# Performance work log

Hardware: AMD Instinct MI355X
Metric: run time of the kernel (lower is better)

Reference implementation:

```python
import jax, jax.numpy as jnp
import numpy as np

WD = WH = WW = 7      # cubic window
NH = 3                # num_heads
RATE = 1              # idx == 1 -> rate = 1, num_heads_rate = 0
FF = 3.0              # focusing_factor (<= 6 branch)
EPS = 1e-6


def setup_inputs() -> dict:
    key = jax.random.key(0)
    ks = jax.random.split(key, 6)
    B, D, H, W, C = 1, 56, 56, 56, 96
    hd = C // NH
    x = jax.random.normal(ks[0], (B, D, H, W, C), dtype=jnp.float32)
    w_qkv = jax.random.normal(ks[1], (C, 3 * C), dtype=jnp.float32) * 0.02
    scale_param = jnp.zeros((RATE, 1, 1, hd), dtype=jnp.float32)
    pos_enc = jax.random.normal(ks[2], (RATE, 1, WD * WH * WW, hd), dtype=jnp.float32) * 0.02
    dwc_w = jax.random.normal(ks[3], (hd * RATE, 1, 5, 5, 5), dtype=jnp.float32) * 0.02
    dwc_b = jnp.zeros((hd * RATE,), dtype=jnp.float32)
    w_proj = jax.random.normal(ks[4], (C, C), dtype=jnp.float32) * 0.02
    b_proj = jnp.zeros((C,), dtype=jnp.float32)
    return {"x": x, "w_qkv": w_qkv, "scale_param": scale_param, "pos_enc": pos_enc,
            "dwc_w": dwc_w, "dwc_b": dwc_b, "w_proj": w_proj, "b_proj": b_proj}


def _forward(x, w_qkv, scale_param, pos_enc, dwc_w, dwc_b, w_proj, b_proj):
    B, D, H, W, C = x.shape
    hd = C // NH
    nD, nH_, nW_ = D // WD, H // WH, W // WW
    N = WD * WH * WW
    # qkv projection (no bias) -> (3, B, D, H, W, C)
    qkv = (x @ w_qkv).reshape(B, D, H, W, 3, C).transpose(4, 0, 1, 2, 3, 5)
    # window partition (rate == 1): (3, 1, B*nWin, N, C)
    qkv = qkv.reshape(3, B, nD, WD, nH_, WH, nW_, WW, C)
    qkv = qkv.transpose(0, 1, 2, 4, 6, 3, 5, 7, 8).reshape(3, RATE, B * nD * nH_ * nW_, N, C)
    q, k, v = qkv[0], qkv[1], qkv[2]

    def heads(t):  # 'r b n (h c) -> r (b h) n c'
        r, b, n, c0 = t.shape
        return t.reshape(r, b, n, NH, hd).transpose(0, 1, 3, 2, 4).reshape(r, b * NH, n, hd)

    q, k, v = heads(q), heads(k), heads(v)
    k = k + pos_enc
    scale = jax.nn.softplus(scale_param)
    q = (jax.nn.relu(q) + EPS) / scale
    k = (jax.nn.relu(k) + EPS) / scale
    qn = jnp.linalg.norm(q, axis=-1, keepdims=True)
    kn = jnp.linalg.norm(k, axis=-1, keepdims=True)
    q = q ** FF
    k = k ** FF
    q = q / jnp.linalg.norm(q, axis=-1, keepdims=True) * qn
    k = k / jnp.linalg.norm(k, axis=-1, keepdims=True) * kn
    # linear attention, kv-first branch (i*j*(c+d) > c*d*(i+j) for N=343, hd=32)
    z = 1.0 / (jnp.einsum('rbic,rbc->rbi', q, k.sum(axis=2)) + EPS)
    kv = jnp.einsum('rbjc,rbjd->rbcd', k, v)
    out = jnp.einsum('rbic,rbcd,rbi->rbid', q, kv, z)
    # depthwise 3D conv feature map on v: 'r b (d w h) c -> b (r c) d w h'
    r, b, n, c = v.shape
    fm = v.reshape(r, b, WD, WH, WW, c).transpose(1, 0, 5, 2, 3, 4).reshape(b, r * c, WD, WH, WW)
    fm = jax.lax.conv_general_dilated(fm, dwc_w, (1, 1, 1), [(2, 2)] * 3,
                                      dimension_numbers=('NCDHW', 'OIDHW', 'NCDHW'),
                                      feature_group_count=r * c)
    fm = fm + dwc_b[None, :, None, None, None]
    fm = fm.reshape(b, r, c, WD, WH, WW).transpose(1, 0, 3, 4, 5, 2).reshape(r, b, n, c)
    out = out + fm
    # merge heads: 'r (b h) n c -> r b n (h c)'
    Bw = b // NH
    out = out.reshape(r, Bw, NH, n, hd).transpose(0, 1, 3, 2, 4).reshape(r, Bw, n, C)
    # window reverse (rate == 1)
    out = out.reshape(B, nD, nH_, nW_, WD, WH, WW, C)
    out = out.transpose(0, 1, 4, 2, 5, 3, 6, 7).reshape(B, D, H, W, C)
    return out @ w_proj + b_proj


def reference(x, w_qkv, scale_param, pos_enc, dwc_w, dwc_b, w_proj, b_proj):
    return _forward(x, w_qkv, scale_param, pos_enc, dwc_w, dwc_b, w_proj, b_proj)
```

## Files before the change

### kernel.cpp

```cpp
#include <hip/hip_runtime.h>
#include <math.h>

#define NWIN 512
#define NHD  3
#define NTOK 343
#define HD   32
#define CH   96
#define DIM  56

#define XS 16.0f
#define WS 1024.0f
#define RS (1.0f/16384.0f)

typedef __attribute__((ext_vector_type(8))) _Float16 f16x8;
typedef __attribute__((ext_vector_type(4))) float f32x4;

__device__ __forceinline__ unsigned short f2h_bits(float x) {
    _Float16 h = (_Float16)x;
    return __builtin_bit_cast(unsigned short, h);
}
__device__ __forceinline__ float h2f_bits(unsigned short u) {
    return (float)__builtin_bit_cast(_Float16, u);
}
__device__ __forceinline__ f32x4 mfma16h(f16x8 a, f16x8 b, f32x4 c) {
    return __builtin_amdgcn_mfma_f32_16x16x32_f16(a, b, c, 0, 0, 0);
}
__device__ __forceinline__ float shfl16_sum(float v) {
    v += __shfl_xor(v, 1);
    v += __shfl_xor(v, 2);
    v += __shfl_xor(v, 4);
    v += __shfl_xor(v, 8);
    return v;
}

__global__ void setup_w(const float* __restrict__ w_qkv,
                        unsigned short* __restrict__ wsb)
{
    int i = blockIdx.x * 256 + threadIdx.x;
    if (i >= 108 * 512) return;
    int e = i & 7, l = (i >> 3) & 63;
    int fid = i >> 9;
    int hl = fid & 1; int f2 = fid >> 1;
    int ks = f2 % 3; int f3 = f2 / 3;
    int nt = f3 & 1; int f4 = f3 >> 1;
    int m  = f4 % 3; int h  = f4 / 3;
    int kg  = ks * 32 + (l >> 4) * 8 + e;
    int col = m * 96 + h * 32 + nt * 16 + (l & 15);
    float w = w_qkv[kg * 288 + col] * WS;
    unsigned short hi = f2h_bits(w);
    wsb[i] = hl ? f2h_bits(w - h2f_bits(hi)) : hi;
}

#define BUILD_AFRAG(AH, AL, XPTR)                                           \
  { _Pragma("unroll")                                                       \
    for (int ks = 0; ks < 3; ++ks) {                                        \
        float4 x0 = *(const float4*)((XPTR) + ks * 32);                     \
        float4 x1 = *(const float4*)((XPTR) + ks * 32 + 4);                 \
        union { _Float16 e[8]; f16x8 v; } th, tl;                           \
        float s[8] = {x0.x, x0.y, x0.z, x0.w, x1.x, x1.y, x1.z, x1.w};      \
        _Pragma("unroll")                                                   \
        for (int e = 0; e < 8; ++e) {                                       \
            float sv = s[e] * XS;                                           \
            unsigned short hi = f2h_bits(sv);                               \
            th.e[e] = __builtin_bit_cast(_Float16, hi);                     \
            tl.e[e] = (_Float16)(sv - h2f_bits(hi));                        \
        }                                                                   \
        AH[ks] = th.v; AL[ks] = tl.v;                                       \
    } }

__global__ __launch_bounds__(256, 4) void attn_kernel(
    const float* __restrict__ x, const unsigned short* __restrict__ wsb,
    const float* __restrict__ scale_param, const float* __restrict__ pos_enc,
    const float* __restrict__ dwc_w, const float* __restrict__ dwc_b,
    float* __restrict__ y)
{
    __shared__ __align__(16) unsigned short v16[352 * HD];
    __shared__ __align__(16) union UU {
        struct PA { unsigned short kf16c[64 * 34]; } pa;
        struct PB {
            unsigned short qfL[64 * 40];
            unsigned short kvS[32 * 40];
            float ksred[4][2][16];
        } pb;
        float dwc[HD * 125];
    } u;
    __shared__ float ksum_s[HD];
    __shared__ float sps[HD];

    const int tid = threadIdx.x, bid = blockIdx.x;
    const int h = bid >> 9, win = bid & 511;
    const int wd = win >> 6, wh = (win >> 3) & 7, ww = win & 7;
    const int wv = tid >> 6, lane = tid & 63;
    const int quad = lane >> 4, li = lane & 15;
    const int g8 = tid >> 5, c = tid & 31;
    const int mtw = wv >> 1, ntw = wv & 1;

    if (tid < HD) {
        float sv = scale_param[tid];
        sps[tid] = (sv > 20.f) ? sv : log1pf(expf(sv));
    }
    __syncthreads();
    const float sp0 = sps[li], sp1 = sps[16 + li];

    const f16x8* wf = (const f16x8*)wsb;
    const int fbase = h * 36;
    float ksp0 = 0.f, ksp1 = 0.f;
    f32x4 kvacc = {0.f, 0.f, 0.f, 0.f};

    for (int cb0 = 0; cb0 < NTOK; cb0 += 64) {
        const int nj = min(64, NTOK - cb0);
        int atok = cb0 + wv * 16 + li;
        int atc = min(atok, NTOK - 1);
        int adz = atc / 49, arem = atc - adz * 49, ady = arem / 7, adx = arem - ady * 7;
        int gA = ((wd * 7 + adz) * DIM + (wh * 7 + ady)) * DIM + (ww * 7 + adx);
        const float* xr = x + (size_t)gA * CH + quad * 8;
        f16x8 ah[3], al[3];
        BUILD_AFRAG(ah, al, xr);

        f32x4 ak[2] = {{0,0,0,0},{0,0,0,0}};
        f32x4 av[2] = {{0,0,0,0},{0,0,0,0}};
        #pragma unroll
        for (int nt = 0; nt < 2; ++nt) {
            #pragma unroll
            for (int ks = 0; ks < 3; ++ks) {
                int fk = (fbase + ((1 * 2 + nt) * 3 + ks) * 2) * 64 + lane;
                int fv = (fbase + ((2 * 2 + nt) * 3 + ks) * 2) * 64 + lane;
                f16x8 bkh = wf[fk], bkl = wf[fk + 64];
                f16x8 bvh = wf[fv];
                ak[nt] = mfma16h(ah[ks], bkh, ak[nt]);
                ak[nt] = mfma16h(ah[ks], bkl, ak[nt]);
                ak[nt] = mfma16h(al[ks], bkh, ak[nt]);
                av[nt] = mfma16h(ah[ks], bvh, av[nt]);
                av[nt] = mfma16h(al[ks], bvh, av[nt]);
            }
        }

        #pragma unroll
        for (int j = 0; j < 4; ++j) {
            int t16 = quad * 4 + j;
            int tok = cb0 + wv * 16 + t16;
            bool val = tok < NTOK;
            int tc = val ? tok : NTOK - 1;
            float pe0 = pos_enc[tc * HD + li];
            float pe1 = pos_enc[tc * HD + 16 + li];
            float kr0 = ak[0][j] * RS + pe0;
            float kr1 = ak[1][j] * RS + pe1;
            float kp0 = (fmaxf(kr0, 0.f) + 1e-6f) / sp0;
            float kp1 = (fmaxf(kr1, 0.f) + 1e-6f) / sp1;
            float k30 = kp0 * kp0 * kp0, k31 = kp1 * kp1 * kp1;
            float n2k = fmaf(kp0, kp0, kp1 * kp1);
            float n6k = fmaf(k30, k30, k31 * k31);
            n2k = shfl16_sum(n2k); n6k = shfl16_sum(n6k);
            float sk = sqrtf(n2k / n6k);
            float kf0 = k30 * sk, kf1 = k31 * sk;
            int tl = wv * 16 + t16;
            if (val) {
                ksp0 += kf0; ksp1 += kf1;
                u.pa.kf16c[tl * 34 + li]      = f2h_bits(kf0);
                u.pa.kf16c[tl * 34 + 16 + li] = f2h_bits(kf1);
                v16[tok * HD + li]      = f2h_bits(av[0][j] * RS);
                v16[tok * HD + 16 + li] = f2h_bits(av[1][j] * RS);
            } else {
                u.pa.kf16c[tl * 34 + li]      = 0;
                u.pa.kf16c[tl * 34 + 16 + li] = 0;
                if (tok < 352) {
                    v16[tok * HD + li]      = 0;
                    v16[tok * HD + 16 + li] = 0;
                }
            }
        }
        __syncthreads();

        const int nsteps = (nj + 31) >> 5;
        for (int s = 0; s < nsteps; ++s) {
            union { unsigned short u16a[8]; f16x8 v; } a8, b8;
            #pragma unroll
            for (int e = 0; e < 8; ++e) {
                int row = s * 32 + quad * 8 + e;
                a8.u16a[e] = u.pa.kf16c[row * 34 + mtw * 16 + li];
                b8.u16a[e] = v16[(cb0 + row) * HD + ntw * 16 + li];
            }
            kvacc = mfma16h(a8.v, b8.v, kvacc);
        }
        __syncthreads();
    }

    ksp0 += __shfl_xor(ksp0, 16); ksp0 += __shfl_xor(ksp0, 32);
    ksp1 += __shfl_xor(ksp1, 16); ksp1 += __shfl_xor(ksp1, 32);
    if (quad == 0) { u.pb.ksred[wv][0][li] = ksp0; u.pb.ksred[wv][1][li] = ksp1; }
    #pragma unroll
    for (int j = 0; j < 4; ++j)
        u.pb.kvS[(ntw * 16 + li) * 40 + mtw * 16 + quad * 4 + j] = f2h_bits(kvacc[j]);
    __syncthreads();
    if (tid < HD) {
        ksum_s[tid] = u.pb.ksred[0][tid >> 4][tid & 15] + u.pb.ksred[1][tid >> 4][tid & 15]
                    + u.pb.ksred[2][tid >> 4][tid & 15] + u.pb.ksred[3][tid >> 4][tid & 15];
    }
    __syncthreads();

    const float ks0 = ksum_s[li], ks1 = ksum_s[16 + li];
    for (int cb0 = 0; cb0 < NTOK; cb0 += 64) {
        int atok = cb0 + wv * 16 + li;
        int atc = min(atok, NTOK - 1);
        int adz = atc / 49, arem = atc - adz * 49, ady = arem / 7, adx = arem - ady * 7;
        int gA = ((wd * 7 + adz) * DIM + (wh * 7 + ady)) * DIM + (ww * 7 + adx);
        const float* xr = x + (size_t)gA * CH + quad * 8;
        f16x8 ah[3], al[3];
        BUILD_AFRAG(ah, al, xr);

        f32x4 aq[2] = {{0,0,0,0},{0,0,0,0}};
        #pragma unroll
        for (int nt = 0; nt < 2; ++nt) {
            #pragma unroll
            for (int ks = 0; ks < 3; ++ks) {
                int fq = (fbase + ((0 * 2 + nt) * 3 + ks) * 2) * 64 + lane;
                f16x8 bqh = wf[fq], bql = wf[fq + 64];
                aq[nt] = mfma16h(ah[ks], bqh, aq[nt]);
                aq[nt] = mfma16h(ah[ks], bql, aq[nt]);
                aq[nt] = mfma16h(al[ks], bqh, aq[nt]);
            }
        }

        float zq[4];
        #pragma unroll
        for (int j = 0; j < 4; ++j) {
            int t16 = quad * 4 + j;
            int tok = cb0 + wv * 16 + t16;
            bool val = tok < NTOK;
            float qp0 = (fmaxf(aq[0][j] * RS, 0.f) + 1e-6f) / sp0;
            float qp1 = (fmaxf(aq[1][j] * RS, 0.f) + 1e-6f) / sp1;
            float q30 = qp0 * qp0 * qp0, q31 = qp1 * qp1 * qp1;
            float n2q = fmaf(qp0, qp0, qp1 * qp1);
            float n6q = fmaf(q30, q30, q31 * q31);
            n2q = shfl16_sum(n2q); n6q = shfl16_sum(n6q);
            float sq = sqrtf(n2q / n6q);
            float qf0 = q30 * sq, qf1 = q31 * sq;
            float zp = shfl16_sum(fmaf(qf0, ks0, qf1 * ks1));
            zq[j] = 1.f / (zp + 1e-6f);
            if (val) {
                int tl = wv * 16 + t16;
                u.pb.qfL[tl * 40 + li]      = f2h_bits(qf0);
                u.pb.qfL[tl * 40 + 16 + li] = f2h_bits(qf1);
            }
        }
        f16x8 aqf = *(const f16x8*)&u.pb.qfL[(wv * 16 + li) * 40 + quad * 8];
        f16x8 bk0 = *(const f16x8*)&u.pb.kvS[li * 40 + quad * 8];
        f16x8 bk1 = *(const f16x8*)&u.pb.kvS[(16 + li) * 40 + quad * 8];
        f32x4 at0 = {0.f, 0.f, 0.f, 0.f}, at1 = {0.f, 0.f, 0.f, 0.f};
        at0 = mfma16h(aqf, bk0, at0);
        at1 = mfma16h(aqf, bk1, at1);

        #pragma unroll
        for (int j = 0; j < 4; ++j) {
            int t16 = quad * 4 + j;
            int tok = cb0 + wv * 16 + t16;
            if (tok < NTOK) {
                int dz = tok / 49, rem = tok - dz * 49, dy = rem / 7, dxx = rem - dy * 7;
                int g = ((wd * 7 + dz) * DIM + (wh * 7 + dy)) * DIM + (ww * 7 + dxx);
                y[(size_t)g * CH + h * HD + li]      = at0[j] * zq[j];
                y[(size_t)g * CH + h * HD + 16 + li] = at1[j] * zq[j];
            }
        }
    }

    __threadfence_block();
    __syncthreads();

    for (int i = tid; i < HD * 125; i += 256) u.dwc[i] = dwc_w[i];
    __syncthreads();

    const float bias_c = dwc_b[c];
    for (int it = g8; it < 49; it += 8) {
        int dz = it / 7, dy = it - dz * 7;
        float fm[7] = {0.f, 0.f, 0.f, 0.f, 0.f, 0.f, 0.f};
        #pragma unroll
        for (int ka2 = 0; ka2 < 5; ++ka2) {
            int za = dz + ka2 - 2;
            if ((unsigned)za >= 7u) continue;
            #pragma unroll
            for (int kb = 0; kb < 5; ++kb) {
                int zb = dy + kb - 2;
                if ((unsigned)zb >= 7u) continue;
                const unsigned short* vb = &v16[(za * 49 + zb * 7) * HD + c];
                float vr[7];
                #pragma unroll
                for (int xx = 0; xx < 7; ++xx) vr[xx] = h2f_bits(vb[xx * HD]);
                const float* wb = &u.dwc[c * 125 + ka2 * 25 + kb * 5];
                float w0 = wb[0], w1 = wb[1], w2 = wb[2], w3 = wb[3], w4 = wb[4];
                #pragma unroll
                for (int dx2 = 0; dx2 < 7; ++dx2) {
                    if (dx2 - 2 >= 0) fm[dx2] = fmaf(vr[dx2 - 2], w0, fm[dx2]);
                    if (dx2 - 1 >= 0) fm[dx2] = fmaf(vr[dx2 - 1], w1, fm[dx2]);
                    fm[dx2] = fmaf(vr[dx2], w2, fm[dx2]);
                    if (dx2 + 1 <= 6) fm[dx2] = fmaf(vr[dx2 + 1], w3, fm[dx2]);
                    if (dx2 + 2 <= 6) fm[dx2] = fmaf(vr[dx2 + 2], w4, fm[dx2]);
                }
            }
        }
        int tokbase = ((wd * 7 + dz) * DIM + (wh * 7 + dy)) * DIM + ww * 7;
        #pragma unroll
        for (int dx2 = 0; dx2 < 7; ++dx2) {
            float* yp = &y[(size_t)(tokbase + dx2) * CH + h * HD + c];
            *yp += fm[dx2] + bias_c;
        }
    }
}

__global__ __launch_bounds__(512, 1) void proj_kernel(
    const float* __restrict__ wp, const float* __restrict__ bp,
    float* __restrict__ y)
{
    __shared__ float yt[256 * 97];
    __shared__ float wl[96 * 96];

    const int tid = threadIdx.x;
    const int base = blockIdx.x * 256;

    for (int i = tid; i < 96 * 96; i += 512) wl[i] = wp[i];
    for (int i = tid; i < 256 * 96; i += 512) {
        int r = i / 96; int ch2 = i - r * 96;
        yt[r * 97 + ch2] = y[(base + r) * 96 + ch2];
    }
    __syncthreads();

    const int tokg = tid & 127;
    const int outg = tid >> 7;

    float acc[2][24];
    #pragma unroll
    for (int jj = 0; jj < 24; ++jj) {
        float b = bp[outg * 24 + jj];
        acc[0][jj] = b; acc[1][jj] = b;
    }

    for (int cc = 0; cc < 96; ++cc) {
        float y0 = yt[(tokg)       * 97 + cc];
        float y1 = yt[(tokg + 128) * 97 + cc];
        const float* wrow = &wl[cc * 96 + outg * 24];
        #pragma unroll
        for (int jj = 0; jj < 24; ++jj) {
            float wvv = wrow[jj];
            acc[0][jj] = fmaf(y0, wvv, acc[0][jj]);
            acc[1][jj] = fmaf(y1, wvv, acc[1][jj]);
        }
    }
    __syncthreads();

    #pragma unroll
    for (int i = 0; i < 2; ++i) {
        int tok = base + tokg + 128 * i;
        #pragma unroll
        for (int jj = 0; jj < 24; ++jj)
            y[tok * 96 + outg * 24 + jj] = acc[i][jj];
    }
}

extern "C" void kernel_launch(void* const* d_in, const int* in_sizes, int n_in,
                              void* d_out, int out_size, void* d_ws, size_t ws_size,
                              hipStream_t stream) {
    const float* x           = (const float*)d_in[0];
    const float* w_qkv       = (const float*)d_in[1];
    const float* scale_param = (const float*)d_in[2];
    const float* pos_enc     = (const float*)d_in[3];
    const float* dwc_w       = (const float*)d_in[4];
    const float* dwc_b       = (const float*)d_in[5];
    const float* w_proj      = (const float*)d_in[6];
    const float* b_proj      = (const float*)d_in[7];
    float* out = (float*)d_out;
    unsigned short* wsb = (unsigned short*)d_ws;

    setup_w<<<dim3(216), dim3(256), 0, stream>>>(w_qkv, wsb);
    attn_kernel<<<dim3(NHD * NWIN), dim3(256), 0, stream>>>(
        x, wsb, scale_param, pos_enc, dwc_w, dwc_b, out);
    proj_kernel<<<dim3(686), dim3(512), 0, stream>>>(w_proj, b_proj, out);
}
```

Measured before the change: 292.4 us.

## Run output projection on MFMA with split-f16 weights prepacked in setup

```diff
diff --git a/kernel.cpp b/kernel.cpp
--- a/kernel.cpp
+++ b/kernel.cpp
@@ -11,6 +11,8 @@
 #define XS 16.0f
 #define WS 1024.0f
 #define RS (1.0f/16384.0f)
+#define YS 4.0f
+#define RSP (1.0f/4096.0f)
 
 typedef __attribute__((ext_vector_type(8))) _Float16 f16x8;
 typedef __attribute__((ext_vector_type(4))) float f32x4;
@@ -34,24 +36,40 @@
 }
 
 __global__ void setup_w(const float* __restrict__ w_qkv,
+                        const float* __restrict__ w_proj,
                         unsigned short* __restrict__ wsb)
 {
     int i = blockIdx.x * 256 + threadIdx.x;
-    if (i >= 108 * 512) return;
+    if (i >= 144 * 512) return;
     int e = i & 7, l = (i >> 3) & 63;
-    int fid = i >> 9;
-    int hl = fid & 1; int f2 = fid >> 1;
-    int ks = f2 % 3; int f3 = f2 / 3;
-    int nt = f3 & 1; int f4 = f3 >> 1;
-    int m  = f4 % 3; int h  = f4 / 3;
-    int kg  = ks * 32 + (l >> 4) * 8 + e;
-    int col = m * 96 + h * 32 + nt * 16 + (l & 15);
-    float w = w_qkv[kg * 288 + col] * WS;
-    unsigned short hi = f2h_bits(w);
-    wsb[i] = hl ? f2h_bits(w - h2f_bits(hi)) : hi;
-}
-
-#define BUILD_AFRAG(AH, AL, XPTR)                                           \
+    int kg, col; const float* src;
+    int fid;
+    if (i < 108 * 512) {
+        fid = i >> 9;
+        int hl = fid & 1; int f2 = fid >> 1;
+        int ks = f2 % 3; int f3 = f2 / 3;
+        int nt = f3 & 1; int f4 = f3 >> 1;
+        int m  = f4 % 3; int h  = f4 / 3;
+        kg  = ks * 32 + (l >> 4) * 8 + e;
+        col = m * 96 + h * 32 + nt * 16 + (l & 15);
+        src = w_qkv; 
+        float w = src[kg * 288 + col] * WS;
+        unsigned short hi = f2h_bits(w);
+        wsb[i] = (fid & 1) ? f2h_bits(w - h2f_bits(hi)) : hi;
+    } else {
+        int i2 = i - 108 * 512;
+        fid = i2 >> 9;
+        int hl = fid & 1; int f2 = fid >> 1;
+        int ks = f2 % 3; int nt = f2 / 3;
+        kg  = ks * 32 + (l >> 4) * 8 + e;
+        col = nt * 16 + (l & 15);
+        float w = w_proj[kg * 96 + col] * WS;
+        unsigned short hi = f2h_bits(w);
+        wsb[i] = hl ? f2h_bits(w - h2f_bits(hi)) : hi;
+    }
+}
+
+#define BUILD_AFRAG_S(AH, AL, XPTR, SCALE)                                  \
   { _Pragma("unroll")                                                       \
     for (int ks = 0; ks < 3; ++ks) {                                        \
         float4 x0 = *(const float4*)((XPTR) + ks * 32);                     \
@@ -60,7 +78,7 @@
         float s[8] = {x0.x, x0.y, x0.z, x0.w, x1.x, x1.y, x1.z, x1.w};      \
         _Pragma("unroll")                                                   \
         for (int e = 0; e < 8; ++e) {                                       \
-            float sv = s[e] * XS;                                           \
+            float sv = s[e] * (SCALE);                                      \
             unsigned short hi = f2h_bits(sv);                               \
             th.e[e] = __builtin_bit_cast(_Float16, hi);                     \
             tl.e[e] = (_Float16)(sv - h2f_bits(hi));                        \
@@ -115,7 +133,7 @@
         int gA = ((wd * 7 + adz) * DIM + (wh * 7 + ady)) * DIM + (ww * 7 + adx);
         const float* xr = x + (size_t)gA * CH + quad * 8;
         f16x8 ah[3], al[3];
-        BUILD_AFRAG(ah, al, xr);
+        BUILD_AFRAG_S(ah, al, xr, XS);
 
         f32x4 ak[2] = {{0,0,0,0},{0,0,0,0}};
         f32x4 av[2] = {{0,0,0,0},{0,0,0,0}};
@@ -206,7 +224,7 @@
         int gA = ((wd * 7 + adz) * DIM + (wh * 7 + ady)) * DIM + (ww * 7 + adx);
         const float* xr = x + (size_t)gA * CH + quad * 8;
         f16x8 ah[3], al[3];
-        BUILD_AFRAG(ah, al, xr);
+        BUILD_AFRAG_S(ah, al, xr, XS);
 
         f32x4 aq[2] = {{0,0,0,0},{0,0,0,0}};
         #pragma unroll
@@ -306,52 +324,44 @@
     }
 }
 
-__global__ __launch_bounds__(512, 1) void proj_kernel(
-    const float* __restrict__ wp, const float* __restrict__ bp,
+__global__ __launch_bounds__(256, 8) void proj_kernel(
+    const unsigned short* __restrict__ wsp, const float* __restrict__ bp,
     float* __restrict__ y)
 {
-    __shared__ float yt[256 * 97];
-    __shared__ float wl[96 * 96];
-
     const int tid = threadIdx.x;
+    const int wv = tid >> 6, lane = tid & 63;
+    const int quad = lane >> 4, li = lane & 15;
     const int base = blockIdx.x * 256;
-
-    for (int i = tid; i < 96 * 96; i += 512) wl[i] = wp[i];
-    for (int i = tid; i < 256 * 96; i += 512) {
-        int r = i / 96; int ch2 = i - r * 96;
-        yt[r * 97 + ch2] = y[(base + r) * 96 + ch2];
-    }
-    __syncthreads();
-
-    const int tokg = tid & 127;
-    const int outg = tid >> 7;
-
-    float acc[2][24];
+    const f16x8* wf = (const f16x8*)wsp;
+
+    float bv[6];
     #pragma unroll
-    for (int jj = 0; jj < 24; ++jj) {
-        float b = bp[outg * 24 + jj];
-        acc[0][jj] = b; acc[1][jj] = b;
-    }
-
-    for (int cc = 0; cc < 96; ++cc) {
-        float y0 = yt[(tokg)       * 97 + cc];
-        float y1 = yt[(tokg + 128) * 97 + cc];
-        const float* wrow = &wl[cc * 96 + outg * 24];
-        #pragma unroll
-        for (int jj = 0; jj < 24; ++jj) {
-            float wvv = wrow[jj];
-            acc[0][jj] = fmaf(y0, wvv, acc[0][jj]);
-            acc[1][jj] = fmaf(y1, wvv, acc[1][jj]);
-        }
-    }
-    __syncthreads();
-
-    #pragma unroll
-    for (int i = 0; i < 2; ++i) {
-        int tok = base + tokg + 128 * i;
-        #pragma unroll
-        for (int jj = 0; jj < 24; ++jj)
-            y[tok * 96 + outg * 24 + jj] = acc[i][jj];
+    for (int nt = 0; nt < 6; ++nt) bv[nt] = bp[nt * 16 + li];
+
+    #pragma unroll 1
+    for (int mt = 0; mt < 4; ++mt) {
+        const int m = wv * 4 + mt;
+        const int tok = base + m * 16 + li;
+        const float* yr = y + (size_t)tok * 96 + quad * 8;
+        f16x8 ah[3], al[3];
+        BUILD_AFRAG_S(ah, al, yr, YS);
+
+        const int rbase = base + m * 16 + quad * 4;
+        #pragma unroll
+        for (int nt = 0; nt < 6; ++nt) {
+            f32x4 acc = {0.f, 0.f, 0.f, 0.f};
+            #pragma unroll
+            for (int ks = 0; ks < 3; ++ks) {
+                int f = ((nt * 3 + ks) * 2) * 64 + lane;
+                f16x8 bh = wf[f], bl = wf[f + 64];
+                acc = mfma16h(ah[ks], bh, acc);
+                acc = mfma16h(ah[ks], bl, acc);
+                acc = mfma16h(al[ks], bh, acc);
+            }
+            #pragma unroll
+            for (int j = 0; j < 4; ++j)
+                y[(size_t)(rbase + j) * 96 + nt * 16 + li] = acc[j] * RSP + bv[nt];
+        }
     }
 }
 
@@ -369,8 +379,9 @@
     float* out = (float*)d_out;
     unsigned short* wsb = (unsigned short*)d_ws;
 
-    setup_w<<<dim3(216), dim3(256), 0, stream>>>(w_qkv, wsb);
+    setup_w<<<dim3(288), dim3(256), 0, stream>>>(w_qkv, w_proj, wsb);
     attn_kernel<<<dim3(NHD * NWIN), dim3(256), 0, stream>>>(
         x, wsb, scale_param, pos_enc, dwc_w, dwc_b, out);
-    proj_kernel<<<dim3(686), dim3(512), 0, stream>>>(w_proj, b_proj, out);
-}
+    proj_kernel<<<dim3(686), dim3(256), 0, stream>>>(
+        wsb + 108 * 512, b_proj, out);
+}
```

Result: slower. 315.4 us (+7.9%).
